# Optimization experiments

Measured on AMD Instinct MI355X. Metric: run time of the kernel, lower is better.

The kernel has to match this reference:

```python
import jax, jax.numpy as jnp
import numpy as np

B, T, D, H, O = 512, 512, 256, 200, 1


def setup_inputs() -> dict:
    key = jax.random.key(0)
    ks = jax.random.split(key, 7)
    s = 1.0 / np.sqrt(H)  # PyTorch LSTM init scale
    x = jax.random.normal(ks[0], (B, T, D), dtype=jnp.float32)
    W_ih = jax.random.uniform(ks[1], (4 * H, D), jnp.float32, -s, s)
    W_hh = jax.random.uniform(ks[2], (4 * H, H), jnp.float32, -s, s)
    b_ih = jax.random.uniform(ks[3], (4 * H,), jnp.float32, -s, s)
    b_hh = jax.random.uniform(ks[4], (4 * H,), jnp.float32, -s, s)
    so = 1.0 / np.sqrt(H * T)
    W_out = jax.random.uniform(ks[5], (O, H * T), jnp.float32, -so, so)
    b_out = jax.random.uniform(ks[6], (O,), jnp.float32, -so, so)
    return {"input_seq": x, "W_ih": W_ih, "W_hh": W_hh, "b_ih": b_ih,
            "b_hh": b_hh, "W_out": W_out, "b_out": b_out}


def _lstm(x, W_ih, W_hh, b_ih, b_hh):
    # Precompute input contribution for all timesteps: [B,T,4H] -> [T,B,4H]
    pre = jnp.einsum('btd,gd->btg', x, W_ih) + b_ih + b_hh
    pre = jnp.transpose(pre, (1, 0, 2))
    h0 = jnp.zeros((x.shape[0], H), x.dtype)
    c0 = jnp.zeros((x.shape[0], H), x.dtype)

    def step(carry, pt):
        h, c = carry
        gates = pt + h @ W_hh.T  # [B,4H]
        i, f, g, o = jnp.split(gates, 4, axis=-1)  # PyTorch gate order i,f,g,o
        i = jax.nn.sigmoid(i)
        f = jax.nn.sigmoid(f)
        g = jnp.tanh(g)
        o = jax.nn.sigmoid(o)
        c_new = f * c + i * g
        h_new = o * jnp.tanh(c_new)
        return (h_new, c_new), h_new

    _, outs = jax.lax.scan(step, (h0, c0), pre)  # outs: [T,B,H]
    return jnp.transpose(outs, (1, 0, 2))  # [B,T,H]


def reference(input_seq, W_ih, W_hh, b_ih, b_hh, W_out, b_out):
    all_outs = _lstm(input_seq, W_ih, W_hh, b_ih, b_hh)  # [B,T,H]
    flat = all_outs.reshape(all_outs.shape[0], -1)  # [B, T*H]
    return flat @ W_out.T + b_out  # [B, O]
```

## Files before the change

kernel.cpp:

```cpp
#include <hip/hip_runtime.h>
#include <hip/hip_bf16.h>

#define B_SZ 512
#define T_SZ 512
#define D_SZ 256
#define H_SZ 200
#define G4   800
#define NSUB 50
#define BS   8
#define WROW 800

typedef __attribute__((ext_vector_type(8))) short short8;
typedef __attribute__((ext_vector_type(4))) short short4v;
typedef __attribute__((ext_vector_type(4))) float f32x4;

__device__ __forceinline__ unsigned short f2bf(float x) {
    unsigned u = __builtin_bit_cast(unsigned, x);
    unsigned r = (u + 0x7FFFu + ((u >> 16) & 1u)) >> 16;
    return (unsigned short)r;
}
__device__ __forceinline__ float sigm(float v) { return 1.f / (1.f + __expf(-v)); }

__device__ __forceinline__ void gl_lds16(const void* g, void* l) {
    __builtin_amdgcn_global_load_lds(
        (const __attribute__((address_space(1))) unsigned int*)g,
        (__attribute__((address_space(3))) unsigned int*)l, 16, 0, 0);
}

__global__ __launch_bounds__(256)
void cvt_bf16(const float* __restrict__ src, unsigned short* __restrict__ dst, int n4)
{
    int i = blockIdx.x * 256 + threadIdx.x;
    const int stride = gridDim.x * 256;
    for (; i < n4; i += stride) {
        float4 v = ((const float4*)src)[i];
        unsigned a = (unsigned)f2bf(v.x) | ((unsigned)f2bf(v.y) << 16);
        unsigned b = (unsigned)f2bf(v.z) | ((unsigned)f2bf(v.w) << 16);
        ((uint2*)dst)[i] = make_uint2(a, b);
    }
}

__global__ __launch_bounds__(256)
void cvt_w_perm(const float* __restrict__ Wih, unsigned short* __restrict__ dst)
{
    int i = blockIdx.x * 256 + threadIdx.x;
    if (i >= G4 * (D_SZ / 4)) return;
    const int r = i >> 6, ch = i & 63;
    const int p = (r & 3) * H_SZ + (r >> 2);
    float4 v = ((const float4*)(Wih + (size_t)p * D_SZ))[ch];
    unsigned a = (unsigned)f2bf(v.x) | ((unsigned)f2bf(v.y) << 16);
    unsigned b = (unsigned)f2bf(v.z) | ((unsigned)f2bf(v.w) << 16);
    ((uint2*)dst)[i] = make_uint2(a, b);
}

__global__ __launch_bounds__(256)
void prep(const float* __restrict__ bih, const float* __restrict__ bhh,
          const float* __restrict__ Wout, float* __restrict__ bsum,
          float* __restrict__ wpad)
{
    const int i = blockIdx.x * 256 + threadIdx.x;
    if (i < G4) {
        const int p = (i & 3) * H_SZ + (i >> 2);
        bsum[i] = bih[p] + bhh[p];
    }
    if (i < T_SZ * H_SZ + 256)
        wpad[i] = (i < T_SZ * H_SZ) ? Wout[i] : 0.f;
}

__global__ __launch_bounds__(256)
void pre_gemm(const unsigned short* __restrict__ xbf,
              const unsigned short* __restrict__ wbf,
              const float* __restrict__ bs,
              unsigned short* __restrict__ pre, int t0)
{
    const int tt = blockIdx.x;
    const int t  = t0 + tt;
    const int b0 = blockIdx.y * 64;
    const int g0 = blockIdx.z * 256;

    __shared__ unsigned short Al[256 * 32];
    __shared__ unsigned short Bl[64 * 32];

    const int tid  = threadIdx.x;
    const int w    = tid >> 6;
    const int lane = tid & 63;
    const int col  = lane & 15, q = lane >> 4;

    f32x4 acc[4][4];
    #pragma unroll
    for (int i = 0; i < 4; ++i)
        #pragma unroll
        for (int j = 0; j < 4; ++j) acc[i][j] = (f32x4)0.f;

    const int arow = w * 64 + (lane >> 2);
    const int akoff = (lane & 3) * 8;
    const int brow = b0 + w * 16 + (lane >> 2);

    for (int kc = 0; kc < 8; ++kc) {
        const int d0 = kc * 32;
        if (kc) __syncthreads();
        #pragma unroll
        for (int j = 0; j < 4; ++j) {
            int g = g0 + arow + j * 16;
            if (g > G4 - 1) g = G4 - 1;
            gl_lds16(wbf + (size_t)g * D_SZ + d0 + akoff,
                     (void*)(Al + (w * 64 + j * 16) * 32));
        }
        gl_lds16(xbf + ((size_t)brow * T_SZ + t) * D_SZ + d0 + akoff,
                 (void*)(Bl + (w * 16) * 32));
        __syncthreads();

        short8 af[4], bv[4];
        #pragma unroll
        for (int s = 0; s < 4; ++s)
            af[s] = *(const short8*)&Al[(w * 64 + s * 16 + col) * 32 + q * 8];
        #pragma unroll
        for (int s = 0; s < 4; ++s)
            bv[s] = *(const short8*)&Bl[(s * 16 + col) * 32 + q * 8];
        #pragma unroll
        for (int gs = 0; gs < 4; ++gs)
            #pragma unroll
            for (int bsi = 0; bsi < 4; ++bsi)
                acc[gs][bsi] = __builtin_amdgcn_mfma_f32_16x16x32_bf16(af[gs], bv[bsi], acc[gs][bsi], 0, 0, 0);
    }

    #pragma unroll
    for (int gs = 0; gs < 4; ++gs) {
        const int S = blockIdx.z * 16 + w * 4 + gs;
        if (S < NSUB) {
            const int gq = S * 16 + q * 4;
            const float4 bi = *(const float4*)&bs[gq];
            #pragma unroll
            for (int bsi = 0; bsi < 4; ++bsi) {
                f32x4 a = acc[gs][bsi];
                unsigned lo = (unsigned)f2bf(a[0] + bi.x) |
                              ((unsigned)f2bf(a[1] + bi.y) << 16);
                unsigned hi = (unsigned)f2bf(a[2] + bi.z) |
                              ((unsigned)f2bf(a[3] + bi.w) << 16);
                const size_t idx = (((size_t)tt * NSUB + S) * 4 + q) * 512 + (b0 + bsi * 16 + col);
                ((uint2*)pre)[idx] = make_uint2(lo, hi);
            }
        }
    }
}

__global__ __launch_bounds__(512, 2)
void lstm_rec(const unsigned short* __restrict__ pre,
              const float* __restrict__ Whh,
              const float* __restrict__ wpad,
              const float* __restrict__ bout,
              float* __restrict__ state,
              float* __restrict__ out,
              int t0, int C_T)
{
    const int bk = blockIdx.x;
    const int cidx = (bk >> 3) + (bk & 7) * 32;
    const int b0 = cidx * 2;

    const int tid = threadIdx.x, lane = tid & 63, wv = tid >> 6;
    const int col = lane & 15, q = lane >> 4;

    __shared__ __align__(16) unsigned short preS[2 * BS * 1600];
    __shared__ __align__(16) short hT[1600];
    __shared__ __align__(16) float woutS[2 * 256];
    __shared__ float redbuf[16];

    const int tbase = (wv < 2) ? wv * 7 : 14 + (wv - 2) * 6;

    int pofs[7], tjv[7];
    #pragma unroll
    for (int j = 0; j < 7; ++j) {
        const int tr = tbase + j;
        const int tj = tr > 49 ? 49 : tr;
        tjv[j] = tj;
        pofs[j] = (tj * 4 + q) * 8 + (col >> 3) * 4;
    }
    const int c7 = col & 7;
    const int jsel = (c7 < 7) ? c7 : 6;
    const bool valid = (wv < 2) ? (c7 < 7) : (c7 < 6);
    const int bsel = col >> 3;
    const int usel = tjv[jsel] * 4 + q;
    const int hw_base = valid ? (bsel * 256 + usel) : (1024 + lane);
    const int rbase = bsel * 256;

    short8 aw[7][6];
#if __has_builtin(__builtin_amdgcn_mfma_f32_16x16x16bf16_1k)
    short4v aw6[7];
#else
    short8 aw6[7];
#endif
    #pragma unroll
    for (int j = 0; j < 7; ++j) {
        const int gp = tjv[j] * 16 + col;
        const float* wr = Whh + (size_t)((gp & 3) * H_SZ + (gp >> 2)) * H_SZ;
        #pragma unroll
        for (int kc = 0; kc < 6; ++kc) {
            const int k = kc * 32 + q * 8;
            float4 f0 = *(const float4*)(wr + k);
            float4 f1 = *(const float4*)(wr + k + 4);
            short8 s;
            s[0] = (short)f2bf(f0.x); s[1] = (short)f2bf(f0.y);
            s[2] = (short)f2bf(f0.z); s[3] = (short)f2bf(f0.w);
            s[4] = (short)f2bf(f1.x); s[5] = (short)f2bf(f1.y);
            s[6] = (short)f2bf(f1.z); s[7] = (short)f2bf(f1.w);
            aw[j][kc] = s;
        }
#if __has_builtin(__builtin_amdgcn_mfma_f32_16x16x16bf16_1k)
        short4v t4 = (short4v)0;
        if (q < 2) {
            float4 f = *(const float4*)(wr + 192 + q * 4);
            t4[0] = (short)f2bf(f.x); t4[1] = (short)f2bf(f.y);
            t4[2] = (short)f2bf(f.z); t4[3] = (short)f2bf(f.w);
        }
        aw6[j] = t4;
#else
        short8 t8 = (short8)0;
        if (q == 0) {
            float4 f0 = *(const float4*)(wr + 192);
            float4 f1 = *(const float4*)(wr + 196);
            t8[0] = (short)f2bf(f0.x); t8[1] = (short)f2bf(f0.y);
            t8[2] = (short)f2bf(f0.z); t8[3] = (short)f2bf(f0.w);
            t8[4] = (short)f2bf(f1.x); t8[5] = (short)f2bf(f1.y);
            t8[6] = (short)f2bf(f1.z); t8[7] = (short)f2bf(f1.w);
        }
        aw6[j] = t8;
#endif
    }

    float* h_st  = state;
    float* c_st  = state + (size_t)B_SZ * H_SZ;
    float* oa_st = state + (size_t)2 * B_SZ * H_SZ;

    for (int i = tid; i < 1600; i += 512) {
        short v = 0;
        if (t0 > 0 && i < 512) {
            const int r = i >> 8, u = i & 255;
            if (u < H_SZ) v = (short)f2bf(h_st[(size_t)(b0 + r) * H_SZ + u]);
        }
        hT[i] = v;
    }

    float c_v = 0.f, oa_v = 0.f;
    if (t0 > 0 && valid) {
        c_v  = c_st [(size_t)(b0 + bsel) * H_SZ + usel];
        oa_v = oa_st[(size_t)(b0 + bsel) * H_SZ + usel];
    }

    const int nblk = C_T / BS;
    const char* preb = (const char*)pre;

    {
        const char* src = preb + ((size_t)wv * 200) * 4096 + (size_t)b0 * 8;
        unsigned short* dst = preS + (0 * BS + wv) * 1600;
        gl_lds16(src + (size_t)lane * 4096,         dst);
        gl_lds16(src + (size_t)(lane + 64) * 4096,  dst + 512);
        gl_lds16(src + (size_t)(lane + 128) * 4096, dst + 1024);
        gl_lds16(src + (size_t)(lane + 136) * 4096, dst + 1088);
    }
    if (wv == 7)
        gl_lds16((const char*)wpad + (size_t)t0 * WROW + lane * 16, (void*)woutS);
    __syncthreads();

    for (int blk = 0; blk < nblk; ++blk) {
        const int bn = blk & 1;
        {
            const int nb = (blk + 1 < nblk) ? blk + 1 : blk;
            const char* src = preb + ((size_t)(nb * BS + wv) * 200) * 4096 + (size_t)b0 * 8;
            unsigned short* dst = preS + ((bn ^ 1) * BS + wv) * 1600;
            gl_lds16(src + (size_t)lane * 4096,         dst);
            gl_lds16(src + (size_t)(lane + 64) * 4096,  dst + 512);
            gl_lds16(src + (size_t)(lane + 128) * 4096, dst + 1024);
            gl_lds16(src + (size_t)(lane + 136) * 4096, dst + 1088);
        }
        const unsigned short* psb = preS + bn * (BS * 1600);

        for (int s = 0; s < BS; ++s) {
            const int tc = blk * BS + s;
            const unsigned short* ps = psb + s * 1600;

            if (wv == 7) {
                int tn = t0 + tc + 1; if (tn > T_SZ - 1) tn = T_SZ - 1;
                gl_lds16((const char*)wpad + (size_t)tn * WROW + lane * 16,
                         (void*)(woutS + ((tc + 1) & 1) * 256));
            }

            const short* hrow = hT + ((tc & 1) << 9) + rbase;

            f32x4 acc[7];
            #pragma unroll
            for (int j = 0; j < 7; ++j) {
                const uint2 p = *(const uint2*)(ps + pofs[j]);
                f32x4 a;
                a[0] = __builtin_bit_cast(float, p.x << 16);
                a[1] = __builtin_bit_cast(float, p.x & 0xFFFF0000u);
                a[2] = __builtin_bit_cast(float, p.y << 16);
                a[3] = __builtin_bit_cast(float, p.y & 0xFFFF0000u);
                acc[j] = a;
            }
            #pragma unroll
            for (int kc = 0; kc < 6; ++kc) {
                const short8 bf = *(const short8*)(hrow + kc * 32 + q * 8);
                #pragma unroll
                for (int j = 0; j < 7; ++j)
                    acc[j] = __builtin_amdgcn_mfma_f32_16x16x32_bf16(aw[j][kc], bf, acc[j], 0, 0, 0);
            }
#if __has_builtin(__builtin_amdgcn_mfma_f32_16x16x16bf16_1k)
            {
                const short4v bt = *(const short4v*)(hrow + 192 + q * 4);
                #pragma unroll
                for (int j = 0; j < 7; ++j)
                    acc[j] = __builtin_amdgcn_mfma_f32_16x16x16bf16_1k(aw6[j], bt, acc[j], 0, 0, 0);
            }
#else
            {
                const short8 bt = *(const short8*)(hrow + 192 + q * 8);
                #pragma unroll
                for (int j = 0; j < 7; ++j)
                    acc[j] = __builtin_amdgcn_mfma_f32_16x16x32_bf16(aw6[j], bt, acc[j], 0, 0, 0);
            }
#endif
            f32x4 sel = acc[0];
            #pragma unroll
            for (int j = 1; j < 7; ++j)
                if (jsel == j) sel = acc[j];

            const float gi = sigm(sel[0]);
            const float gf = sigm(sel[1]);
            const float gg = 2.f * sigm(2.f * sel[2]) - 1.f;
            const float go = sigm(sel[3]);
            const float cn = gf * c_v + gi * gg;
            c_v = cn;
            const float hv = go * (2.f * sigm(2.f * cn) - 1.f);
            oa_v += hv * woutS[(tc & 1) * 256 + usel];
            hT[hw_base + (((tc + 1) & 1) << 9)] = (short)f2bf(hv);
            if (t0 + C_T < T_SZ && tc == C_T - 1 && valid)
                h_st[(size_t)(b0 + bsel) * H_SZ + usel] = hv;
            __syncthreads();
        }
    }

    if (t0 + C_T >= T_SZ) {
        float v = valid ? oa_v : 0.f;
        v += __shfl_xor(v, 1);
        v += __shfl_xor(v, 2);
        v += __shfl_xor(v, 4);
        v += __shfl_xor(v, 16);
        v += __shfl_xor(v, 32);
        if (lane == 0) redbuf[wv * 2]     = v;
        if (lane == 8) redbuf[wv * 2 + 1] = v;
        __syncthreads();
        if (tid < 2) {
            float r = bout[0];
            #pragma unroll
            for (int w = 0; w < 8; ++w) r += redbuf[w * 2 + tid];
            out[b0 + tid] = r;
        }
    } else if (valid) {
        c_st [(size_t)(b0 + bsel) * H_SZ + usel] = c_v;
        oa_st[(size_t)(b0 + bsel) * H_SZ + usel] = oa_v;
    }
}

extern "C" void kernel_launch(void* const* d_in, const int* in_sizes, int n_in,
                              void* d_out, int out_size, void* d_ws, size_t ws_size,
                              hipStream_t stream)
{
    const float* x    = (const float*)d_in[0];
    const float* Wih  = (const float*)d_in[1];
    const float* Whh  = (const float*)d_in[2];
    const float* bih  = (const float*)d_in[3];
    const float* bhh  = (const float*)d_in[4];
    const float* Wout = (const float*)d_in[5];
    const float* bout = (const float*)d_in[6];
    float* out = (float*)d_out;

    char* ws = (char*)d_ws;
    float* state = (float*)ws;
    size_t off = (size_t)3 * B_SZ * H_SZ * sizeof(float);
    float* bsum = (float*)(ws + off);
    off += (size_t)G4 * sizeof(float);
    float* wpad = (float*)(ws + off);
    off += (size_t)(T_SZ * H_SZ + 256) * sizeof(float);
    unsigned short* xbf = (unsigned short*)(ws + off);
    off += (size_t)B_SZ * T_SZ * D_SZ * 2;
    unsigned short* wbf = (unsigned short*)(ws + off);
    off += (size_t)G4 * D_SZ * 2;
    unsigned short* pre = (unsigned short*)(ws + off);

    const size_t per_t = (size_t)NSUB * 4 * 512 * 4 * 2;
    int ct = 512;
    while (ct > BS && off + (size_t)ct * per_t > ws_size) ct >>= 1;

    cvt_bf16<<<dim3(2048), dim3(256), 0, stream>>>(x, xbf, B_SZ * T_SZ * D_SZ / 4);
    cvt_w_perm<<<dim3(200), dim3(256), 0, stream>>>(Wih, wbf);
    prep<<<dim3(402), dim3(256), 0, stream>>>(bih, bhh, Wout, bsum, wpad);

    for (int t0 = 0; t0 < T_SZ; t0 += ct) {
        pre_gemm<<<dim3(ct, 8, 4), dim3(256), 0, stream>>>(
            xbf, wbf, bsum, pre, t0);
        lstm_rec<<<dim3(256), dim3(512), 0, stream>>>(
            pre, Whh, wpad, bout, state, out, t0, ct);
    }
}
```

Baseline: 1.638 ms.

## Move part of W_hh tiles to LDS and rebalance gate tiles across waves

The recurrent kernel now keeps five 16-row W_hh tiles per wave in registers and stages the remaining ten tiles in LDS, so that the 50 tiles are spread evenly (5 per wave, plus shared extras) instead of 7/6 per wave. The aim is to cut VGPR pressure and improve load balance, at the cost of extra LDS reads of A fragments every step. W_out rows are now prefetched one block at a time alongside the pre-activations, replacing the per-step single-wave load. Intra-block barriers become a raw s_barrier with an lgkmcnt wait, and the full __syncthreads is kept only at block boundaries. The raw barrier relies on the LDS-only dependencies within the block being covered by that wait.

Result: slower. 1.672 ms (+2.0%).

```diff
diff --git a/kernel.cpp b/kernel.cpp
--- a/kernel.cpp
+++ b/kernel.cpp
@@ -9,6 +9,7 @@
 #define NSUB 50
 #define BS   8
 #define WROW 800
+#define WAT  216
 
 typedef __attribute__((ext_vector_type(8))) short short8;
 typedef __attribute__((ext_vector_type(4))) short short4v;
@@ -161,37 +162,53 @@
     const int col = lane & 15, q = lane >> 4;
 
     __shared__ __align__(16) unsigned short preS[2 * BS * 1600];
+    __shared__ __align__(16) unsigned short wA[10 * 16 * WAT];
     __shared__ __align__(16) short hT[1600];
-    __shared__ __align__(16) float woutS[2 * 256];
+    __shared__ __align__(16) float woutS[2 * BS * 256];
     __shared__ float redbuf[16];
 
-    const int tbase = (wv < 2) ? wv * 7 : 14 + (wv - 2) * 6;
-
-    int pofs[7], tjv[7];
+    const int c7 = col & 7;
+    const int bsel = col >> 3;
+    const int rbase = bsel * 256;
+
+    const int own = (c7 < 5) ? (wv * 5 + c7) : ((c7 == 5) ? (40 + wv) : (48 + (wv & 1)));
+    const bool valid = (c7 < 6) || (c7 == 6 && wv < 2);
+    const int usel = own * 4 + q;
+    const int hw_base = valid ? (bsel * 256 + usel) : (1024 + lane);
+    const int jsel = (c7 < 7) ? c7 : 6;
+
+    int pofs[7];
     #pragma unroll
-    for (int j = 0; j < 7; ++j) {
-        const int tr = tbase + j;
-        const int tj = tr > 49 ? 49 : tr;
-        tjv[j] = tj;
-        pofs[j] = (tj * 4 + q) * 8 + (col >> 3) * 4;
-    }
-    const int c7 = col & 7;
-    const int jsel = (c7 < 7) ? c7 : 6;
-    const bool valid = (wv < 2) ? (c7 < 7) : (c7 < 6);
-    const int bsel = col >> 3;
-    const int usel = tjv[jsel] * 4 + q;
-    const int hw_base = valid ? (bsel * 256 + usel) : (1024 + lane);
-    const int rbase = bsel * 256;
-
-    short8 aw[7][6];
+    for (int j = 0; j < 5; ++j)
+        pofs[j] = ((wv * 5 + j) * 4 + q) * 8 + bsel * 4;
+    pofs[5] = ((40 + wv) * 4 + q) * 8 + bsel * 4;
+    pofs[6] = ((48 + (wv & 1)) * 4 + q) * 8 + bsel * 4;
+
+    for (int idx = tid; idx < 10 * 16 * 50; idx += 512) {
+        const int L = idx / 800;
+        const int rem = idx - L * 800;
+        const int r = rem / 50;
+        const int kq = rem - r * 50;
+        const int gp = (40 + L) * 16 + r;
+        const float4 f = *(const float4*)(Whh + (size_t)((gp & 3) * H_SZ + (gp >> 2)) * H_SZ + kq * 4);
+        unsigned lo = (unsigned)f2bf(f.x) | ((unsigned)f2bf(f.y) << 16);
+        unsigned hi = (unsigned)f2bf(f.z) | ((unsigned)f2bf(f.w) << 16);
+        *(uint2*)(wA + (size_t)L * 16 * WAT + r * WAT + kq * 4) = make_uint2(lo, hi);
+    }
+    for (int idx = tid; idx < 160 * 16; idx += 512) {
+        const int row = idx >> 4;
+        wA[row * WAT + 200 + (idx & 15)] = 0;
+    }
+
+    short8 aw[5][6];
 #if __has_builtin(__builtin_amdgcn_mfma_f32_16x16x16bf16_1k)
-    short4v aw6[7];
+    short4v aw6[5];
 #else
-    short8 aw6[7];
+    short8 aw6[5];
 #endif
     #pragma unroll
-    for (int j = 0; j < 7; ++j) {
-        const int gp = tjv[j] * 16 + col;
+    for (int j = 0; j < 5; ++j) {
+        const int gp = (wv * 5 + j) * 16 + col;
         const float* wr = Whh + (size_t)((gp & 3) * H_SZ + (gp >> 2)) * H_SZ;
         #pragma unroll
         for (int kc = 0; kc < 6; ++kc) {
@@ -227,6 +244,11 @@
 #endif
     }
 
+    const unsigned short* wA5  = wA + (size_t)wv * 16 * WAT + col * WAT + q * 8;
+    const unsigned short* wA6  = wA + (size_t)(8 + (wv & 1)) * 16 * WAT + col * WAT + q * 8;
+    const unsigned short* wA5t = wA + (size_t)wv * 16 * WAT + col * WAT + 192 + q * 4;
+    const unsigned short* wA6t = wA + (size_t)(8 + (wv & 1)) * 16 * WAT + col * WAT + 192 + q * 4;
+
     float* h_st  = state;
     float* c_st  = state + (size_t)B_SZ * H_SZ;
     float* oa_st = state + (size_t)2 * B_SZ * H_SZ;
@@ -256,9 +278,9 @@
         gl_lds16(src + (size_t)(lane + 64) * 4096,  dst + 512);
         gl_lds16(src + (size_t)(lane + 128) * 4096, dst + 1024);
         gl_lds16(src + (size_t)(lane + 136) * 4096, dst + 1088);
-    }
-    if (wv == 7)
-        gl_lds16((const char*)wpad + (size_t)t0 * WROW + lane * 16, (void*)woutS);
+        gl_lds16((const char*)wpad + (size_t)(t0 + wv) * WROW + lane * 16,
+                 (void*)(woutS + wv * 256));
+    }
     __syncthreads();
 
     for (int blk = 0; blk < nblk; ++blk) {
@@ -271,19 +293,14 @@
             gl_lds16(src + (size_t)(lane + 64) * 4096,  dst + 512);
             gl_lds16(src + (size_t)(lane + 128) * 4096, dst + 1024);
             gl_lds16(src + (size_t)(lane + 136) * 4096, dst + 1088);
+            gl_lds16((const char*)wpad + (size_t)(t0 + nb * BS + wv) * WROW + lane * 16,
+                     (void*)(woutS + ((bn ^ 1) * BS + wv) * 256));
         }
         const unsigned short* psb = preS + bn * (BS * 1600);
 
         for (int s = 0; s < BS; ++s) {
             const int tc = blk * BS + s;
             const unsigned short* ps = psb + s * 1600;
-
-            if (wv == 7) {
-                int tn = t0 + tc + 1; if (tn > T_SZ - 1) tn = T_SZ - 1;
-                gl_lds16((const char*)wpad + (size_t)tn * WROW + lane * 16,
-                         (void*)(woutS + ((tc + 1) & 1) * 256));
-            }
-
             const short* hrow = hT + ((tc & 1) << 9) + rbase;
 
             f32x4 acc[7];
@@ -300,23 +317,41 @@
             #pragma unroll
             for (int kc = 0; kc < 6; ++kc) {
                 const short8 bf = *(const short8*)(hrow + kc * 32 + q * 8);
+                const short8 a5 = *(const short8*)(wA5 + kc * 32);
                 #pragma unroll
-                for (int j = 0; j < 7; ++j)
+                for (int j = 0; j < 5; ++j)
                     acc[j] = __builtin_amdgcn_mfma_f32_16x16x32_bf16(aw[j][kc], bf, acc[j], 0, 0, 0);
+                acc[5] = __builtin_amdgcn_mfma_f32_16x16x32_bf16(a5, bf, acc[5], 0, 0, 0);
+                if (wv < 2) {
+                    const short8 a6 = *(const short8*)(wA6 + kc * 32);
+                    acc[6] = __builtin_amdgcn_mfma_f32_16x16x32_bf16(a6, bf, acc[6], 0, 0, 0);
+                }
             }
 #if __has_builtin(__builtin_amdgcn_mfma_f32_16x16x16bf16_1k)
             {
                 const short4v bt = *(const short4v*)(hrow + 192 + q * 4);
                 #pragma unroll
-                for (int j = 0; j < 7; ++j)
+                for (int j = 0; j < 5; ++j)
                     acc[j] = __builtin_amdgcn_mfma_f32_16x16x16bf16_1k(aw6[j], bt, acc[j], 0, 0, 0);
+                const short4v a5t = *(const short4v*)wA5t;
+                acc[5] = __builtin_amdgcn_mfma_f32_16x16x16bf16_1k(a5t, bt, acc[5], 0, 0, 0);
+                if (wv < 2) {
+                    const short4v a6t = *(const short4v*)wA6t;
+                    acc[6] = __builtin_amdgcn_mfma_f32_16x16x16bf16_1k(a6t, bt, acc[6], 0, 0, 0);
+                }
             }
 #else
             {
                 const short8 bt = *(const short8*)(hrow + 192 + q * 8);
                 #pragma unroll
-                for (int j = 0; j < 7; ++j)
+                for (int j = 0; j < 5; ++j)
                     acc[j] = __builtin_amdgcn_mfma_f32_16x16x32_bf16(aw6[j], bt, acc[j], 0, 0, 0);
+                short8 a5t = (q == 0) ? *(const short8*)(wA5t) : (short8)0;
+                acc[5] = __builtin_amdgcn_mfma_f32_16x16x32_bf16(a5t, bt, acc[5], 0, 0, 0);
+                if (wv < 2) {
+                    short8 a6t = (q == 0) ? *(const short8*)(wA6t) : (short8)0;
+                    acc[6] = __builtin_amdgcn_mfma_f32_16x16x32_bf16(a6t, bt, acc[6], 0, 0, 0);
+                }
             }
 #endif
             f32x4 sel = acc[0];
@@ -331,11 +366,15 @@
             const float cn = gf * c_v + gi * gg;
             c_v = cn;
             const float hv = go * (2.f * sigm(2.f * cn) - 1.f);
-            oa_v += hv * woutS[(tc & 1) * 256 + usel];
+            oa_v += hv * woutS[(bn * BS + s) * 256 + usel];
             hT[hw_base + (((tc + 1) & 1) << 9)] = (short)f2bf(hv);
             if (t0 + C_T < T_SZ && tc == C_T - 1 && valid)
                 h_st[(size_t)(b0 + bsel) * H_SZ + usel] = hv;
-            __syncthreads();
+
+            if (s == BS - 1)
+                __syncthreads();
+            else
+                asm volatile("s_waitcnt lgkmcnt(0)\n\ts_barrier" ::: "memory");
         }
     }
 
```

## Retile pre_gemm to 512 threads and prefetch recurrence operands across steps

Applied to the files above, without the earlier changes.

pre_gemm now uses 512-thread blocks covering 128 batch rows with a 2x4 wave grid, so each W_ih tile loaded into LDS is reused across twice as many batch rows. In lstm_rec the W_out slices for a whole block of 8 timesteps are staged into LDS alongside the pre-activation prefetch, replacing the per-step load by one wave. The next step's pre-activations and W_out value are read into registers before the barrier, which becomes a raw waitcnt+s_barrier. This aims to take LDS read latency off the serial recurrence path, at the cost of more registers and LDS.

After: 1.667 ms. Within noise of the previous version (+1.8%).

```diff
diff --git a/kernel.cpp b/kernel.cpp
--- a/kernel.cpp
+++ b/kernel.cpp
@@ -67,7 +67,7 @@
         wpad[i] = (i < T_SZ * H_SZ) ? Wout[i] : 0.f;
 }
 
-__global__ __launch_bounds__(256)
+__global__ __launch_bounds__(512)
 void pre_gemm(const unsigned short* __restrict__ xbf,
               const unsigned short* __restrict__ wbf,
               const float* __restrict__ bs,
@@ -75,16 +75,18 @@
 {
     const int tt = blockIdx.x;
     const int t  = t0 + tt;
-    const int b0 = blockIdx.y * 64;
+    const int b0 = blockIdx.y * 128;
     const int g0 = blockIdx.z * 256;
 
     __shared__ unsigned short Al[256 * 32];
-    __shared__ unsigned short Bl[64 * 32];
+    __shared__ unsigned short Bl[128 * 32];
 
     const int tid  = threadIdx.x;
-    const int w    = tid >> 6;
+    const int wv   = tid >> 6;
     const int lane = tid & 63;
     const int col  = lane & 15, q = lane >> 4;
+    const int wm   = wv >> 1;
+    const int wn   = wv & 1;
 
     f32x4 acc[4][4];
     #pragma unroll
@@ -92,31 +94,33 @@
         #pragma unroll
         for (int j = 0; j < 4; ++j) acc[i][j] = (f32x4)0.f;
 
-    const int arow = w * 64 + (lane >> 2);
-    const int akoff = (lane & 3) * 8;
-    const int brow = b0 + w * 16 + (lane >> 2);
+    const int arow_l = lane >> 2;
+    const int akoff  = (lane & 3) * 8;
 
     for (int kc = 0; kc < 8; ++kc) {
         const int d0 = kc * 32;
         if (kc) __syncthreads();
         #pragma unroll
-        for (int j = 0; j < 4; ++j) {
-            int g = g0 + arow + j * 16;
+        for (int j = 0; j < 2; ++j) {
+            int g = g0 + wv * 32 + j * 16 + arow_l;
             if (g > G4 - 1) g = G4 - 1;
             gl_lds16(wbf + (size_t)g * D_SZ + d0 + akoff,
-                     (void*)(Al + (w * 64 + j * 16) * 32));
-        }
-        gl_lds16(xbf + ((size_t)brow * T_SZ + t) * D_SZ + d0 + akoff,
-                 (void*)(Bl + (w * 16) * 32));
+                     (void*)(Al + (wv * 32 + j * 16) * 32));
+        }
+        {
+            const int brow = b0 + wv * 16 + arow_l;
+            gl_lds16(xbf + ((size_t)brow * T_SZ + t) * D_SZ + d0 + akoff,
+                     (void*)(Bl + (wv * 16) * 32));
+        }
         __syncthreads();
 
         short8 af[4], bv[4];
         #pragma unroll
         for (int s = 0; s < 4; ++s)
-            af[s] = *(const short8*)&Al[(w * 64 + s * 16 + col) * 32 + q * 8];
+            af[s] = *(const short8*)&Al[(wm * 64 + s * 16 + col) * 32 + q * 8];
         #pragma unroll
         for (int s = 0; s < 4; ++s)
-            bv[s] = *(const short8*)&Bl[(s * 16 + col) * 32 + q * 8];
+            bv[s] = *(const short8*)&Bl[(wn * 64 + s * 16 + col) * 32 + q * 8];
         #pragma unroll
         for (int gs = 0; gs < 4; ++gs)
             #pragma unroll
@@ -126,7 +130,7 @@
 
     #pragma unroll
     for (int gs = 0; gs < 4; ++gs) {
-        const int S = blockIdx.z * 16 + w * 4 + gs;
+        const int S = blockIdx.z * 16 + wm * 4 + gs;
         if (S < NSUB) {
             const int gq = S * 16 + q * 4;
             const float4 bi = *(const float4*)&bs[gq];
@@ -137,7 +141,8 @@
                               ((unsigned)f2bf(a[1] + bi.y) << 16);
                 unsigned hi = (unsigned)f2bf(a[2] + bi.z) |
                               ((unsigned)f2bf(a[3] + bi.w) << 16);
-                const size_t idx = (((size_t)tt * NSUB + S) * 4 + q) * 512 + (b0 + bsi * 16 + col);
+                const size_t idx = (((size_t)tt * NSUB + S) * 4 + q) * 512 +
+                                   (b0 + wn * 64 + bsi * 16 + col);
                 ((uint2*)pre)[idx] = make_uint2(lo, hi);
             }
         }
@@ -162,7 +167,7 @@
 
     __shared__ __align__(16) unsigned short preS[2 * BS * 1600];
     __shared__ __align__(16) short hT[1600];
-    __shared__ __align__(16) float woutS[2 * 256];
+    __shared__ __align__(16) float woutS[2 * BS * 256];
     __shared__ float redbuf[16];
 
     const int tbase = (wv < 2) ? wv * 7 : 14 + (wv - 2) * 6;
@@ -256,9 +261,9 @@
         gl_lds16(src + (size_t)(lane + 64) * 4096,  dst + 512);
         gl_lds16(src + (size_t)(lane + 128) * 4096, dst + 1024);
         gl_lds16(src + (size_t)(lane + 136) * 4096, dst + 1088);
-    }
-    if (wv == 7)
-        gl_lds16((const char*)wpad + (size_t)t0 * WROW + lane * 16, (void*)woutS);
+        gl_lds16((const char*)wpad + (size_t)(t0 + wv) * WROW + lane * 16,
+                 (void*)(woutS + wv * 256));
+    }
     __syncthreads();
 
     for (int blk = 0; blk < nblk; ++blk) {
@@ -271,30 +276,30 @@
             gl_lds16(src + (size_t)(lane + 64) * 4096,  dst + 512);
             gl_lds16(src + (size_t)(lane + 128) * 4096, dst + 1024);
             gl_lds16(src + (size_t)(lane + 136) * 4096, dst + 1088);
+            gl_lds16((const char*)wpad + (size_t)(t0 + nb * BS + wv) * WROW + lane * 16,
+                     (void*)(woutS + ((bn ^ 1) * BS + wv) * 256));
         }
         const unsigned short* psb = preS + bn * (BS * 1600);
 
+        uint2 pr[7];
+        #pragma unroll
+        for (int j = 0; j < 7; ++j)
+            pr[j] = *(const uint2*)(psb + pofs[j]);
+        float wout_c = woutS[(bn * BS) * 256 + usel];
+
+        #pragma unroll
         for (int s = 0; s < BS; ++s) {
             const int tc = blk * BS + s;
-            const unsigned short* ps = psb + s * 1600;
-
-            if (wv == 7) {
-                int tn = t0 + tc + 1; if (tn > T_SZ - 1) tn = T_SZ - 1;
-                gl_lds16((const char*)wpad + (size_t)tn * WROW + lane * 16,
-                         (void*)(woutS + ((tc + 1) & 1) * 256));
-            }
-
             const short* hrow = hT + ((tc & 1) << 9) + rbase;
 
             f32x4 acc[7];
             #pragma unroll
             for (int j = 0; j < 7; ++j) {
-                const uint2 p = *(const uint2*)(ps + pofs[j]);
                 f32x4 a;
-                a[0] = __builtin_bit_cast(float, p.x << 16);
-                a[1] = __builtin_bit_cast(float, p.x & 0xFFFF0000u);
-                a[2] = __builtin_bit_cast(float, p.y << 16);
-                a[3] = __builtin_bit_cast(float, p.y & 0xFFFF0000u);
+                a[0] = __builtin_bit_cast(float, pr[j].x << 16);
+                a[1] = __builtin_bit_cast(float, pr[j].x & 0xFFFF0000u);
+                a[2] = __builtin_bit_cast(float, pr[j].y << 16);
+                a[3] = __builtin_bit_cast(float, pr[j].y & 0xFFFF0000u);
                 acc[j] = a;
             }
             #pragma unroll
@@ -331,11 +336,20 @@
             const float cn = gf * c_v + gi * gg;
             c_v = cn;
             const float hv = go * (2.f * sigm(2.f * cn) - 1.f);
-            oa_v += hv * woutS[(tc & 1) * 256 + usel];
+            oa_v += hv * wout_c;
             hT[hw_base + (((tc + 1) & 1) << 9)] = (short)f2bf(hv);
             if (t0 + C_T < T_SZ && tc == C_T - 1 && valid)
                 h_st[(size_t)(b0 + bsel) * H_SZ + usel] = hv;
-            __syncthreads();
+
+            if (s < BS - 1) {
+                #pragma unroll
+                for (int j = 0; j < 7; ++j)
+                    pr[j] = *(const uint2*)(psb + (s + 1) * 1600 + pofs[j]);
+                wout_c = woutS[(bn * BS + s + 1) * 256 + usel];
+                asm volatile("s_waitcnt lgkmcnt(0)\n\ts_barrier" ::: "memory");
+            } else {
+                __syncthreads();
+            }
         }
     }
 
@@ -396,7 +410,7 @@
     prep<<<dim3(402), dim3(256), 0, stream>>>(bih, bhh, Wout, bsum, wpad);
 
     for (int t0 = 0; t0 < T_SZ; t0 += ct) {
-        pre_gemm<<<dim3(ct, 8, 4), dim3(256), 0, stream>>>(
+        pre_gemm<<<dim3(ct, 4, 4), dim3(512), 0, stream>>>(
             xbf, wbf, bsum, pre, t0);
         lstm_rec<<<dim3(256), dim3(512), 0, stream>>>(
             pre, Whh, wpad, bout, state, out, t0, ct);
```
